# Kernel tuning notes

Hardware: AMD Instinct MI355X
Metric: run time of the kernel (lower is better)

## Reference

```python
import jax, jax.numpy as jnp
import numpy as np
from jax import lax

N = 100000      # number of nodes (== ninput)
E = 3200000     # number of edges per adjacency
NHID = 128
EPS = 1e-12     # torch F.normalize eps


def spmm(src, dst, w, x):
    # sparse adj @ x : out[i] = sum_{e: dst[e]==i} w[e] * x[src[e]]
    return jax.ops.segment_sum(w[:, None] * x[src], dst, num_segments=N)


def l2norm(x):
    # F.normalize(x, p=2, dim=1)
    n = jnp.sqrt(jnp.sum(x * x, axis=1, keepdims=True))
    return x / jnp.maximum(n, EPS)


def mlp(x, L1, bl1, L2, bl2, L3, bl3):
    # dropout == 0.0 -> identity; chunking is a memory optimization, same math
    h = jax.nn.relu(x @ L1 + bl1)
    h = jax.nn.relu(h @ L2 + bl2)
    return h @ L3 + bl3  # [N, 1]


def setup_inputs() -> dict:
    key = jax.random.key(0)
    ks = jax.random.split(key, 32)
    d = {}
    d["adj1_src"] = jax.random.randint(ks[0], (E,), 0, N, dtype=jnp.int32)
    d["adj1_dst"] = jax.random.randint(ks[1], (E,), 0, N, dtype=jnp.int32)
    d["adj1_w"] = jax.random.uniform(ks[2], (E,), dtype=jnp.float32)
    d["adj2_src"] = jax.random.randint(ks[3], (E,), 0, N, dtype=jnp.int32)
    d["adj2_dst"] = jax.random.randint(ks[4], (E,), 0, N, dtype=jnp.int32)
    d["adj2_w"] = jax.random.uniform(ks[5], (E,), dtype=jnp.float32)
    d["W1"] = jax.random.normal(ks[6], (N, NHID), dtype=jnp.float32) * 0.05
    d["b1"] = jnp.zeros((NHID,), jnp.float32)
    for i, k in zip(range(2, 7), ks[7:12]):
        d[f"W{i}"] = jax.random.normal(k, (NHID, NHID), dtype=jnp.float32) * (1.0 / np.sqrt(NHID))
        d[f"b{i}"] = jnp.zeros((NHID,), jnp.float32)
    d["L1"] = jax.random.normal(ks[12], (NHID, 2 * NHID), dtype=jnp.float32) * (1.0 / np.sqrt(NHID))
    d["bl1"] = jnp.zeros((2 * NHID,), jnp.float32)
    d["L2"] = jax.random.normal(ks[13], (2 * NHID, 2 * NHID), dtype=jnp.float32) * (1.0 / np.sqrt(2 * NHID))
    d["bl2"] = jnp.zeros((2 * NHID,), jnp.float32)
    d["L3"] = jax.random.normal(ks[14], (2 * NHID, 1), dtype=jnp.float32) * (1.0 / np.sqrt(2 * NHID))
    d["bl3"] = jnp.zeros((1,), jnp.float32)
    return d


def reference(adj1_src, adj1_dst, adj1_w, adj2_src, adj2_dst, adj2_w,
              W1, b1, W2, b2, W3, b3, W4, b4, W5, b5, W6, b6,
              L1, bl1, L2, bl2, L3, bl3):
    def branch(src, dst, w):
        x1 = l2norm(jax.nn.relu(spmm(src, dst, w, W1) + b1))
        x2 = l2norm(jax.nn.relu(spmm(src, dst, w, x1 @ W2) + b2))
        x3 = l2norm(jax.nn.relu(spmm(src, dst, w, x2 @ W3) + b3))
        x4 = l2norm(jax.nn.relu(spmm(src, dst, w, x3 @ W4) + b4))
        x5 = l2norm(jax.nn.relu(spmm(src, dst, w, x4 @ W5) + b5))
        x6 = jax.nn.relu(spmm(src, dst, w, x5 @ W6) + b6)
        x7 = lax.stop_gradient(x1 + x2 + x3 + x4 + x5 + x6)  # .detach()
        s = jnp.zeros((N, 1), jnp.float32)
        for xi in (x1, x2, x3, x4, x5):  # computed under torch.no_grad()
            s = s + lax.stop_gradient(mlp(xi, L1, bl1, L2, bl2, L3, bl3))
        s = s + mlp(x6, L1, bl1, L2, bl2, L3, bl3)
        s = s + mlp(x7, L1, bl1, L2, bl2, L3, bl3)
        return s / 7.0

    score1 = branch(adj1_src, adj1_dst, adj1_w)
    score2 = branch(adj2_src, adj2_dst, adj2_w)
    return score1 * score2
```

## Files before the change

### kernel.cpp

```cpp
#include <hip/hip_runtime.h>

#define NN 100000
#define NE 3200000
#define HID 128
#define NNH ((size_t)NN * HID)
#define CAPB 72
#define SP 13
#define FGRID 27097
#define CHE 533504
#define WROWS2 12500
#define GE8 1563

typedef __attribute__((ext_vector_type(8))) _Float16 f16x8;
typedef __attribute__((ext_vector_type(4))) _Float16 f16x4;
typedef __attribute__((ext_vector_type(4))) float f32x4;

#define SWZ(row, k) ((k) ^ (((row) & 7) << 3))

__global__ void zero_k(int* p, int n) {
    int i = blockIdx.x * 256 + threadIdx.x;
    if (i < n) p[i] = 0;
}

__global__ void scatter_xcd_k(const int* __restrict__ src, const int* __restrict__ dst,
                              const float* __restrict__ w, int* __restrict__ cnt,
                              unsigned* __restrict__ ep) {
    int wdx = blockIdx.x & 7;
    int grp = blockIdx.x >> 3;
    int lo = wdx * WROWS2;
    int hi = lo + WROWS2; if (hi > NN) hi = NN;
#pragma unroll
    for (int k = 0; k < 8; ++k) {
        int e = (grp + k * GE8) * 256 + threadIdx.x;
        if (e < NE) {
            int d = dst[e];
            if (d >= lo && d < hi) {
                int pos = atomicAdd(&cnt[d], 1);
                if (pos < CAPB) {
                    ushort hb = __builtin_bit_cast(ushort, (_Float16)w[e]);
                    ep[(size_t)d * CAPB + pos] = ((unsigned)src[e] << 15) | (unsigned)hb;
                }
            }
        }
    }
}

__global__ void convT_k(const float* __restrict__ W, _Float16* __restrict__ WT, int K, int N) {
    int idx = blockIdx.x * 256 + threadIdx.x;
    if (idx < K * N) {
        int k = idx / N, n = idx % N;
        WT[n * K + k] = (_Float16)W[idx];
    }
}

__global__ void conv4_k(const float* __restrict__ A, _Float16* __restrict__ B, int n4) {
    int i = blockIdx.x * 256 + threadIdx.x;
    if (i < n4) {
        float4 v = ((const float4*)A)[i];
        f16x4 h;
        h.x = (_Float16)v.x; h.y = (_Float16)v.y; h.z = (_Float16)v.z; h.w = (_Float16)v.w;
        ((f16x4*)B)[i] = h;
    }
}

template <bool EPI>
__device__ inline void spmm_rows4(const _Float16* __restrict__ x, const int* __restrict__ cnt,
                                  const unsigned* __restrict__ ep, const float* __restrict__ bias,
                                  _Float16* __restrict__ outx, int row0) {
    int l = threadIdx.x & 63;
    int q = l >> 4, li = l & 15;
    int row = row0 + (threadIdx.x >> 6);
    if (row >= NN) return;
    int e0 = row * CAPB;
    int deg = cnt[row];
    if (deg > CAPB) deg = CAPB;
    int e1 = e0 + deg;
    float acc[8] = {};
#pragma unroll 4
    for (int e = e0 + q; e < e1; e += 4) {
        unsigned r = ep[e];
        int s = r >> 15;
        float w = (float)__builtin_bit_cast(_Float16, (ushort)(r & 0x7FFFu));
        f16x8 v = *(const f16x8*)(x + (size_t)s * HID + li * 8);
#pragma unroll
        for (int j = 0; j < 8; ++j) acc[j] += w * (float)v[j];
    }
#pragma unroll
    for (int j = 0; j < 8; ++j) {
        acc[j] += __shfl_xor(acc[j], 16, 64);
        acc[j] += __shfl_xor(acc[j], 32, 64);
    }
    if (EPI) {
        const float4* bp = (const float4*)(bias + li * 8);
        float4 b0 = bp[0], b1 = bp[1];
        acc[0] = fmaxf(acc[0] + b0.x, 0.f); acc[1] = fmaxf(acc[1] + b0.y, 0.f);
        acc[2] = fmaxf(acc[2] + b0.z, 0.f); acc[3] = fmaxf(acc[3] + b0.w, 0.f);
        acc[4] = fmaxf(acc[4] + b1.x, 0.f); acc[5] = fmaxf(acc[5] + b1.y, 0.f);
        acc[6] = fmaxf(acc[6] + b1.z, 0.f); acc[7] = fmaxf(acc[7] + b1.w, 0.f);
        float ss = 0.f;
#pragma unroll
        for (int j = 0; j < 8; ++j) ss += acc[j] * acc[j];
        ss += __shfl_xor(ss, 1, 64);
        ss += __shfl_xor(ss, 2, 64);
        ss += __shfl_xor(ss, 4, 64);
        ss += __shfl_xor(ss, 8, 64);
        float sc = 1.0f / fmaxf(sqrtf(ss), 1e-12f);
#pragma unroll
        for (int j = 0; j < 8; ++j) acc[j] *= sc;
    }
    if (q == 0) {
        f16x8 ho;
#pragma unroll
        for (int j = 0; j < 8; ++j) ho[j] = (_Float16)acc[j];
        *(f16x8*)(outx + (size_t)row * HID + li * 8) = ho;
    }
}

template <bool EPI>
__global__ void spmm_k(const _Float16* __restrict__ x, const int* __restrict__ cnt,
                       const unsigned* __restrict__ ep, const float* __restrict__ bias,
                       _Float16* __restrict__ outx) {
    spmm_rows4<EPI>(x, cnt, ep, bias, outx, blockIdx.x * 4);
}

template <bool EPI>
__global__ void spmm_sc_k(const _Float16* __restrict__ x, const int* __restrict__ cnt,
                          const unsigned* __restrict__ ep, const float* __restrict__ bias,
                          _Float16* __restrict__ outx,
                          const int* __restrict__ src2, const int* __restrict__ dst2,
                          const float* __restrict__ w2, int* __restrict__ cnt2,
                          unsigned* __restrict__ ep2, int ebase) {
    int b = blockIdx.x;
    if (b % SP == SP - 1) {
        int e = ebase + (b / SP) * 256 + threadIdx.x;
        if (e < NE) {
            int d = dst2[e];
            int pos = atomicAdd(&cnt2[d], 1);
            if (pos < CAPB) {
                ushort hb = __builtin_bit_cast(ushort, (_Float16)w2[e]);
                ep2[(size_t)d * CAPB + pos] = ((unsigned)src2[e] << 15) | (unsigned)hb;
            }
        }
        return;
    }
    int mIdx = b - b / SP;
    spmm_rows4<EPI>(x, cnt, ep, bias, outx, mIdx * 4);
}

template <bool NORM>
__global__ __launch_bounds__(256) void trans_mlp_k(
    const _Float16* Y, const _Float16* __restrict__ WT,
    const float* __restrict__ bw, _Float16* Xo,
    const _Float16* __restrict__ L1T, const float* __restrict__ bl1,
    const _Float16* __restrict__ L2T, const float* __restrict__ bl2,
    const float* __restrict__ L3, const float* __restrict__ bl3,
    float* __restrict__ sacc) {
    __shared__ _Float16 Xs[64][128];
    __shared__ _Float16 H1s[64][256];
    __shared__ float red[4][64];
    int t = threadIdx.x;
    int w = t >> 6, l = t & 63;
    int g = l >> 4, li = l & 15;
    int rowBase = blockIdx.x * 64;

#pragma unroll
    for (int i = 0; i < 4; ++i) {
        int idx = t + i * 256;
        int r = idx >> 4, c8 = idx & 15;
        int gr = rowBase + r;
        f16x8 v = (gr < NN) ? *(const f16x8*)(Y + (size_t)gr * 128 + c8 * 8)
                            : (f16x8)(_Float16)0.f;
        *(f16x8*)&Xs[r][SWZ(r, c8 * 8)] = v;
    }
    __syncthreads();

    int cW = w * 32;
    f32x4 accw[4][2] = {};
#pragma unroll
    for (int ks = 0; ks < 4; ++ks) {
        int kb = ks * 32 + g * 8;
        f16x8 a[4];
#pragma unroll
        for (int mt = 0; mt < 4; ++mt) {
            int r = mt * 16 + li;
            a[mt] = *(const f16x8*)&Xs[r][SWZ(r, kb)];
        }
#pragma unroll
        for (int nt = 0; nt < 2; ++nt) {
            f16x8 b = *(const f16x8*)(WT + (size_t)(cW + nt * 16 + li) * 128 + kb);
#pragma unroll
            for (int mt = 0; mt < 4; ++mt)
                accw[mt][nt] = __builtin_amdgcn_mfma_f32_16x16x32_f16(a[mt], b, accw[mt][nt], 0, 0, 0);
        }
    }
    float vv[4][2][4];
    float b0 = bw[cW + li], b1v = bw[cW + 16 + li];
#pragma unroll
    for (int mt = 0; mt < 4; ++mt)
#pragma unroll
        for (int r4 = 0; r4 < 4; ++r4) {
            vv[mt][0][r4] = fmaxf(accw[mt][0][r4] + b0, 0.f);
            vv[mt][1][r4] = fmaxf(accw[mt][1][r4] + b1v, 0.f);
        }
    if (NORM) {
#pragma unroll
        for (int mt = 0; mt < 4; ++mt)
#pragma unroll
            for (int r4 = 0; r4 < 4; ++r4) {
                float ps = vv[mt][0][r4] * vv[mt][0][r4] + vv[mt][1][r4] * vv[mt][1][r4];
                ps += __shfl_xor(ps, 1, 64);
                ps += __shfl_xor(ps, 2, 64);
                ps += __shfl_xor(ps, 4, 64);
                ps += __shfl_xor(ps, 8, 64);
                if (li == 0) red[w][mt * 16 + g * 4 + r4] = ps;
            }
        __syncthreads();
        if (t < 64) {
            float s = red[0][t] + red[1][t] + red[2][t] + red[3][t];
            red[0][t] = 1.f / fmaxf(sqrtf(s), 1e-12f);
        }
        __syncthreads();
    } else {
        __syncthreads();
    }
#pragma unroll
    for (int mt = 0; mt < 4; ++mt)
#pragma unroll
        for (int r4 = 0; r4 < 4; ++r4) {
            int row = mt * 16 + g * 4 + r4;
            float sc = NORM ? red[0][row] : 1.f;
            _Float16 h0 = (_Float16)(vv[mt][0][r4] * sc);
            _Float16 h1 = (_Float16)(vv[mt][1][r4] * sc);
            Xs[row][SWZ(row, cW + li)] = h0;
            Xs[row][SWZ(row, cW + 16 + li)] = h1;
            int gr = rowBase + row;
            if (gr < NN) {
                Xo[(size_t)gr * 128 + cW + li] = h0;
                Xo[(size_t)gr * 128 + cW + 16 + li] = h1;
            }
        }
    __syncthreads();

    int cM = w * 64;
    f32x4 acc[4][4] = {};
#pragma unroll
    for (int ks = 0; ks < 4; ++ks) {
        int kb = ks * 32 + g * 8;
        f16x8 a[4];
#pragma unroll
        for (int mt = 0; mt < 4; ++mt) {
            int r = mt * 16 + li;
            a[mt] = *(const f16x8*)&Xs[r][SWZ(r, kb)];
        }
#pragma unroll
        for (int nt = 0; nt < 4; ++nt) {
            int n = cM + nt * 16 + li;
            f16x8 b = *(const f16x8*)(L1T + (size_t)n * 128 + kb);
#pragma unroll
            for (int mt = 0; mt < 4; ++mt)
                acc[mt][nt] = __builtin_amdgcn_mfma_f32_16x16x32_f16(a[mt], b, acc[mt][nt], 0, 0, 0);
        }
    }
#pragma unroll
    for (int nt = 0; nt < 4; ++nt) {
        int col = cM + nt * 16 + li;
        float bb = bl1[col];
#pragma unroll
        for (int mt = 0; mt < 4; ++mt)
#pragma unroll
            for (int r4 = 0; r4 < 4; ++r4) {
                int row = mt * 16 + g * 4 + r4;
                H1s[row][SWZ(row, col)] = (_Float16)fmaxf(acc[mt][nt][r4] + bb, 0.f);
            }
    }
    __syncthreads();

    f32x4 acc2[4][4] = {};
#pragma unroll
    for (int ks = 0; ks < 8; ++ks) {
        int kb = ks * 32 + g * 8;
        f16x8 a[4];
#pragma unroll
        for (int mt = 0; mt < 4; ++mt) {
            int r = mt * 16 + li;
            a[mt] = *(const f16x8*)&H1s[r][SWZ(r, kb)];
        }
#pragma unroll
        for (int nt = 0; nt < 4; ++nt) {
            int n = cM + nt * 16 + li;
            f16x8 b = *(const f16x8*)(L2T + (size_t)n * 256 + kb);
#pragma unroll
            for (int mt = 0; mt < 4; ++mt)
                acc2[mt][nt] = __builtin_amdgcn_mfma_f32_16x16x32_f16(a[mt], b, acc2[mt][nt], 0, 0, 0);
        }
    }
    float part[4][4] = {};
#pragma unroll
    for (int nt = 0; nt < 4; ++nt) {
        int col = cM + nt * 16 + li;
        float bb = bl2[col];
        float l3v = L3[col];
#pragma unroll
        for (int mt = 0; mt < 4; ++mt)
#pragma unroll
            for (int r4 = 0; r4 < 4; ++r4)
                part[mt][r4] += fmaxf(acc2[mt][nt][r4] + bb, 0.f) * l3v;
    }
#pragma unroll
    for (int mt = 0; mt < 4; ++mt)
#pragma unroll
        for (int r4 = 0; r4 < 4; ++r4) {
            float p = part[mt][r4];
            p += __shfl_xor(p, 1, 64);
            p += __shfl_xor(p, 2, 64);
            p += __shfl_xor(p, 4, 64);
            p += __shfl_xor(p, 8, 64);
            if (li == 0) red[w][mt * 16 + g * 4 + r4] = p;
        }
    __syncthreads();
    if (t < 64) {
        int gr = rowBase + t;
        if (gr < NN)
            sacc[gr] += red[0][t] + red[1][t] + red[2][t] + red[3][t] + bl3[0];
    }
}

template <bool SUM6, bool INIT>
__global__ __launch_bounds__(256) void mlp_fused_k(
    const _Float16* __restrict__ X,
    const _Float16* __restrict__ L1T, const float* __restrict__ bl1,
    const _Float16* __restrict__ L2T, const float* __restrict__ bl2,
    const float* __restrict__ L3, const float* __restrict__ bl3,
    float* __restrict__ sacc) {
    __shared__ _Float16 Xs[64][128];
    __shared__ _Float16 H1s[64][256];
    __shared__ float red[4][64];
    int t = threadIdx.x;
    int w = t >> 6, l = t & 63;
    int g = l >> 4, li = l & 15;
    int rowBase = blockIdx.x * 64;

#pragma unroll
    for (int i = 0; i < 4; ++i) {
        int idx = t + i * 256;
        int r = idx >> 4, c8 = idx & 15;
        int gr = rowBase + r;
        if (SUM6) {
            float s[8] = {};
            if (gr < NN) {
#pragma unroll
                for (int l6 = 0; l6 < 6; ++l6) {
                    f16x8 v = *(const f16x8*)(X + (size_t)l6 * NNH + (size_t)gr * HID + c8 * 8);
#pragma unroll
                    for (int j = 0; j < 8; ++j) s[j] += (float)v[j];
                }
            }
            f16x8 hv;
#pragma unroll
            for (int j = 0; j < 8; ++j) hv[j] = (_Float16)s[j];
            *(f16x8*)&Xs[r][SWZ(r, c8 * 8)] = hv;
        } else {
            f16x8 v = (gr < NN) ? *(const f16x8*)(X + (size_t)gr * HID + c8 * 8)
                                : (f16x8)(_Float16)0.f;
            *(f16x8*)&Xs[r][SWZ(r, c8 * 8)] = v;
        }
    }
    __syncthreads();

    int cM = w * 64;
    f32x4 acc[4][4] = {};
#pragma unroll
    for (int ks = 0; ks < 4; ++ks) {
        int kb = ks * 32 + g * 8;
        f16x8 a[4];
#pragma unroll
        for (int mt = 0; mt < 4; ++mt) {
            int r = mt * 16 + li;
            a[mt] = *(const f16x8*)&Xs[r][SWZ(r, kb)];
        }
#pragma unroll
        for (int nt = 0; nt < 4; ++nt) {
            int n = cM + nt * 16 + li;
            f16x8 b = *(const f16x8*)(L1T + (size_t)n * 128 + kb);
#pragma unroll
            for (int mt = 0; mt < 4; ++mt)
                acc[mt][nt] = __builtin_amdgcn_mfma_f32_16x16x32_f16(a[mt], b, acc[mt][nt], 0, 0, 0);
        }
    }
#pragma unroll
    for (int nt = 0; nt < 4; ++nt) {
        int col = cM + nt * 16 + li;
        float bb = bl1[col];
#pragma unroll
        for (int mt = 0; mt < 4; ++mt)
#pragma unroll
            for (int r4 = 0; r4 < 4; ++r4) {
                int row = mt * 16 + g * 4 + r4;
                H1s[row][SWZ(row, col)] = (_Float16)fmaxf(acc[mt][nt][r4] + bb, 0.f);
            }
    }
    __syncthreads();

    f32x4 acc2[4][4] = {};
#pragma unroll
    for (int ks = 0; ks < 8; ++ks) {
        int kb = ks * 32 + g * 8;
        f16x8 a[4];
#pragma unroll
        for (int mt = 0; mt < 4; ++mt) {
            int r = mt * 16 + li;
            a[mt] = *(const f16x8*)&H1s[r][SWZ(r, kb)];
        }
#pragma unroll
        for (int nt = 0; nt < 4; ++nt) {
            int n = cM + nt * 16 + li;
            f16x8 b = *(const f16x8*)(L2T + (size_t)n * 256 + kb);
#pragma unroll
            for (int mt = 0; mt < 4; ++mt)
                acc2[mt][nt] = __builtin_amdgcn_mfma_f32_16x16x32_f16(a[mt], b, acc2[mt][nt], 0, 0, 0);
        }
    }
    float part[4][4] = {};
#pragma unroll
    for (int nt = 0; nt < 4; ++nt) {
        int col = cM + nt * 16 + li;
        float bb = bl2[col];
        float l3v = L3[col];
#pragma unroll
        for (int mt = 0; mt < 4; ++mt)
#pragma unroll
            for (int r4 = 0; r4 < 4; ++r4)
                part[mt][r4] += fmaxf(acc2[mt][nt][r4] + bb, 0.f) * l3v;
    }
#pragma unroll
    for (int mt = 0; mt < 4; ++mt)
#pragma unroll
        for (int r4 = 0; r4 < 4; ++r4) {
            float p = part[mt][r4];
            p += __shfl_xor(p, 1, 64);
            p += __shfl_xor(p, 2, 64);
            p += __shfl_xor(p, 4, 64);
            p += __shfl_xor(p, 8, 64);
            if (li == 0) red[w][mt * 16 + g * 4 + r4] = p;
        }
    __syncthreads();
    if (t < 64) {
        int gr = rowBase + t;
        if (gr < NN) {
            float s = red[0][t] + red[1][t] + red[2][t] + red[3][t] + bl3[0];
            if (INIT) sacc[gr] = s; else sacc[gr] += s;
        }
    }
}

__global__ void score_store_k(const float* __restrict__ sacc, float* __restrict__ dst) {
    int i = blockIdx.x * 256 + threadIdx.x;
    if (i < NN) dst[i] = sacc[i] * (1.f / 7.f);
}

__global__ void final_mul_k(const float* __restrict__ sacc, const float* __restrict__ score1,
                            float* __restrict__ out) {
    int i = blockIdx.x * 256 + threadIdx.x;
    if (i < NN) out[i] = score1[i] * (sacc[i] * (1.f / 7.f));
}

extern "C" void kernel_launch(void* const* d_in, const int* in_sizes, int n_in,
                              void* d_out, int out_size, void* d_ws, size_t ws_size,
                              hipStream_t stream) {
    const int* asrc[2] = {(const int*)d_in[0], (const int*)d_in[3]};
    const int* adst[2] = {(const int*)d_in[1], (const int*)d_in[4]};
    const float* aw[2] = {(const float*)d_in[2], (const float*)d_in[5]};
    const float* W1 = (const float*)d_in[6];
    const float* b1 = (const float*)d_in[7];
    const float* Wk[5] = {(const float*)d_in[8], (const float*)d_in[10], (const float*)d_in[12],
                          (const float*)d_in[14], (const float*)d_in[16]};
    const float* bk[5] = {(const float*)d_in[9], (const float*)d_in[11], (const float*)d_in[13],
                          (const float*)d_in[15], (const float*)d_in[17]};
    const float* L1 = (const float*)d_in[18];
    const float* bl1 = (const float*)d_in[19];
    const float* L2 = (const float*)d_in[20];
    const float* bl2 = (const float*)d_in[21];
    const float* L3 = (const float*)d_in[22];
    const float* bl3 = (const float*)d_in[23];
    float* out = (float*)d_out;

    char* p = (char*)d_ws;
    _Float16* L1T = (_Float16*)p; p += 65536;
    _Float16* L2T = (_Float16*)p; p += 131072;
    _Float16* WkT = (_Float16*)p; p += 163840;
    _Float16* W1h = (_Float16*)p; p += NNH * 2;
    _Float16* xbuf = (_Float16*)p; p += 6 * NNH * 2;
    float* sacc = (float*)p; p += (size_t)NN * 4;
    float* score1 = (float*)p; p += (size_t)NN * 4;
    unsigned* ep1 = (unsigned*)p; p += (size_t)NN * CAPB * 4;
    unsigned* ep2 = (unsigned*)p; p += (size_t)NN * CAPB * 4;
    int* cnt1 = (int*)p; p += (size_t)NN * 4;
    int* cnt2 = (int*)p; p += (size_t)NN * 4;

    const int GE = (NE + 255) / 256;
    const int GN = (NN + 255) / 256;
    const int GS = (NN + 3) / 4;
    const int GM = (NN + 63) / 64;

    convT_k<<<(128 * 256 + 255) / 256, 256, 0, stream>>>(L1, L1T, 128, 256);
    convT_k<<<(256 * 256 + 255) / 256, 256, 0, stream>>>(L2, L2T, 256, 256);
    for (int l = 0; l < 5; ++l)
        convT_k<<<(128 * 128 + 255) / 256, 256, 0, stream>>>(Wk[l], WkT + (size_t)l * 16384, 128, 128);
    conv4_k<<<(NN * HID / 4 + 255) / 256, 256, 0, stream>>>(W1, W1h, NN * HID / 4);
    zero_k<<<GN, 256, 0, stream>>>(cnt1, NN);
    zero_k<<<GN, 256, 0, stream>>>(cnt2, NN);

    scatter_xcd_k<<<8 * GE8, 256, 0, stream>>>(asrc[0], adst[0], aw[0], cnt1, ep1);

    spmm_sc_k<true><<<FGRID, 256, 0, stream>>>(W1h, cnt1, ep1, b1, xbuf,
                                               asrc[1], adst[1], aw[1], cnt2, ep2, 0);
    mlp_fused_k<false, true><<<GM, 256, 0, stream>>>(xbuf, L1T, bl1, L2T, bl2, L3, bl3, sacc);

    for (int l = 0; l < 5; ++l) {
        _Float16* xo = xbuf + (size_t)(l + 1) * NNH;
        spmm_sc_k<false><<<FGRID, 256, 0, stream>>>(xbuf + (size_t)l * NNH, cnt1, ep1, b1, xo,
                                                    asrc[1], adst[1], aw[1], cnt2, ep2,
                                                    (l + 1) * CHE);
        if (l < 4)
            trans_mlp_k<true><<<GM, 256, 0, stream>>>(xo, WkT + (size_t)l * 16384, bk[l], xo,
                                                      L1T, bl1, L2T, bl2, L3, bl3, sacc);
        else
            trans_mlp_k<false><<<GM, 256, 0, stream>>>(xo, WkT + (size_t)l * 16384, bk[l], xo,
                                                       L1T, bl1, L2T, bl2, L3, bl3, sacc);
    }
    mlp_fused_k<true, false><<<GM, 256, 0, stream>>>(xbuf, L1T, bl1, L2T, bl2, L3, bl3, sacc);
    score_store_k<<<GN, 256, 0, stream>>>(sacc, score1);

    spmm_k<true><<<GS, 256, 0, stream>>>(W1h, cnt2, ep2, b1, xbuf);
    mlp_fused_k<false, true><<<GM, 256, 0, stream>>>(xbuf, L1T, bl1, L2T, bl2, L3, bl3, sacc);
    for (int l = 0; l < 5; ++l) {
        _Float16* xo = xbuf + (size_t)(l + 1) * NNH;
        spmm_k<false><<<GS, 256, 0, stream>>>(xbuf + (size_t)l * NNH, cnt2, ep2, b1, xo);
        if (l < 4)
            trans_mlp_k<true><<<GM, 256, 0, stream>>>(xo, WkT + (size_t)l * 16384, bk[l], xo,
                                                      L1T, bl1, L2T, bl2, L3, bl3, sacc);
        else
            trans_mlp_k<false><<<GM, 256, 0, stream>>>(xo, WkT + (size_t)l * 16384, bk[l], xo,
                                                       L1T, bl1, L2T, bl2, L3, bl3, sacc);
    }
    mlp_fused_k<true, false><<<GM, 256, 0, stream>>>(xbuf, L1T, bl1, L2T, bl2, L3, bl3, sacc);
    final_mul_k<<<GN, 256, 0, stream>>>(sacc, score1, out);
}
```

Measured before the change: 2.471 ms.

## Overlap per-layer MLP scoring with next SpMM via interleaved block roles

Moves the MLP scoring of each layer's normalized features out of the transform kernel and into the following SpMM launch, interleaving MLP blocks with SpMM (and adjacency-scatter) blocks by block-index modulo. The transform kernel becomes a lighter trans_k that only does the matmul, bias, relu and normalize. This removes the separate first MLP launch and lets the compute-heavy MLP overlap with the memory-bound gather. In exchange, grid sizing and role mapping get more complex, and shared memory for the MLP now constrains occupancy of the SpMM blocks.

```diff
diff --git a/kernel.cpp b/kernel.cpp
--- a/kernel.cpp
+++ b/kernel.cpp
@@ -10,6 +10,9 @@
 #define CHE 533504
 #define WROWS2 12500
 #define GE8 1563
+#define GM 1563
+#define G1 28692
+#define G2 26571
 
 typedef __attribute__((ext_vector_type(8))) _Float16 f16x8;
 typedef __attribute__((ext_vector_type(4))) _Float16 f16x4;
@@ -116,6 +119,115 @@
     }
 }
 
+__device__ inline void mlp_body(const _Float16* __restrict__ X, int rowBase,
+                                const _Float16* __restrict__ L1T, const float* __restrict__ bl1,
+                                const _Float16* __restrict__ L2T, const float* __restrict__ bl2,
+                                const float* __restrict__ L3, const float* __restrict__ bl3,
+                                float* __restrict__ sacc, int initF) {
+    __shared__ _Float16 Xs[64][128];
+    __shared__ _Float16 H1s[64][256];
+    __shared__ float red[4][64];
+    int t = threadIdx.x;
+    int w = t >> 6, l = t & 63;
+    int g = l >> 4, li = l & 15;
+
+#pragma unroll
+    for (int i = 0; i < 4; ++i) {
+        int idx = t + i * 256;
+        int r = idx >> 4, c8 = idx & 15;
+        int gr = rowBase + r;
+        f16x8 v = (gr < NN) ? *(const f16x8*)(X + (size_t)gr * HID + c8 * 8)
+                            : (f16x8)(_Float16)0.f;
+        *(f16x8*)&Xs[r][SWZ(r, c8 * 8)] = v;
+    }
+    __syncthreads();
+
+    int cM = w * 64;
+    f32x4 acc[4][4] = {};
+#pragma unroll
+    for (int ks = 0; ks < 4; ++ks) {
+        int kb = ks * 32 + g * 8;
+        f16x8 a[4];
+#pragma unroll
+        for (int mt = 0; mt < 4; ++mt) {
+            int r = mt * 16 + li;
+            a[mt] = *(const f16x8*)&Xs[r][SWZ(r, kb)];
+        }
+#pragma unroll
+        for (int nt = 0; nt < 4; ++nt) {
+            int n = cM + nt * 16 + li;
+            f16x8 b = *(const f16x8*)(L1T + (size_t)n * 128 + kb);
+#pragma unroll
+            for (int mt = 0; mt < 4; ++mt)
+                acc[mt][nt] = __builtin_amdgcn_mfma_f32_16x16x32_f16(a[mt], b, acc[mt][nt], 0, 0, 0);
+        }
+    }
+#pragma unroll
+    for (int nt = 0; nt < 4; ++nt) {
+        int col = cM + nt * 16 + li;
+        float bb = bl1[col];
+#pragma unroll
+        for (int mt = 0; mt < 4; ++mt)
+#pragma unroll
+            for (int r4 = 0; r4 < 4; ++r4) {
+                int row = mt * 16 + g * 4 + r4;
+                H1s[row][SWZ(row, col)] = (_Float16)fmaxf(acc[mt][nt][r4] + bb, 0.f);
+            }
+    }
+    __syncthreads();
+
+    f32x4 acc2[4][4] = {};
+#pragma unroll
+    for (int ks = 0; ks < 8; ++ks) {
+        int kb = ks * 32 + g * 8;
+        f16x8 a[4];
+#pragma unroll
+        for (int mt = 0; mt < 4; ++mt) {
+            int r = mt * 16 + li;
+            a[mt] = *(const f16x8*)&H1s[r][SWZ(r, kb)];
+        }
+#pragma unroll
+        for (int nt = 0; nt < 4; ++nt) {
+            int n = cM + nt * 16 + li;
+            f16x8 b = *(const f16x8*)(L2T + (size_t)n * 256 + kb);
+#pragma unroll
+            for (int mt = 0; mt < 4; ++mt)
+                acc2[mt][nt] = __builtin_amdgcn_mfma_f32_16x16x32_f16(a[mt], b, acc2[mt][nt], 0, 0, 0);
+        }
+    }
+    float part[4][4] = {};
+#pragma unroll
+    for (int nt = 0; nt < 4; ++nt) {
+        int col = cM + nt * 16 + li;
+        float bb = bl2[col];
+        float l3v = L3[col];
+#pragma unroll
+        for (int mt = 0; mt < 4; ++mt)
+#pragma unroll
+            for (int r4 = 0; r4 < 4; ++r4)
+                part[mt][r4] += fmaxf(acc2[mt][nt][r4] + bb, 0.f) * l3v;
+    }
+#pragma unroll
+    for (int mt = 0; mt < 4; ++mt)
+#pragma unroll
+        for (int r4 = 0; r4 < 4; ++r4) {
+            float p = part[mt][r4];
+            p += __shfl_xor(p, 1, 64);
+            p += __shfl_xor(p, 2, 64);
+            p += __shfl_xor(p, 4, 64);
+            p += __shfl_xor(p, 8, 64);
+            if (li == 0) red[w][mt * 16 + g * 4 + r4] = p;
+        }
+    __syncthreads();
+    if (t < 64) {
+        int gr = rowBase + t;
+        if (gr < NN) {
+            float s = red[0][t] + red[1][t] + red[2][t] + red[3][t] + bl3[0];
+            if (initF) sacc[gr] = s; else sacc[gr] += s;
+        }
+    }
+}
+
 template <bool EPI>
 __global__ void spmm_k(const _Float16* __restrict__ x, const int* __restrict__ cnt,
                        const unsigned* __restrict__ ep, const float* __restrict__ bias,
@@ -147,6 +259,143 @@
     spmm_rows4<EPI>(x, cnt, ep, bias, outx, mIdx * 4);
 }
 
+__global__ __launch_bounds__(256) void fused3_k(
+    const _Float16* __restrict__ x, const int* __restrict__ cnt,
+    const unsigned* __restrict__ ep, _Float16* __restrict__ outx,
+    const int* __restrict__ src2, const int* __restrict__ dst2,
+    const float* __restrict__ w2, int* __restrict__ cnt2,
+    unsigned* __restrict__ ep2, int ebase,
+    const _Float16* __restrict__ Xp, int initF,
+    const _Float16* __restrict__ L1T, const float* __restrict__ bl1,
+    const _Float16* __restrict__ L2T, const float* __restrict__ bl2,
+    const float* __restrict__ L3, const float* __restrict__ bl3,
+    float* __restrict__ sacc) {
+    int b = blockIdx.x;
+    int m18 = b % 18;
+    if (m18 == 9) {
+        int midx = b / 18;
+        if (midx < GM) mlp_body(Xp, midx * 64, L1T, bl1, L2T, bl2, L3, bl3, sacc, initF);
+        return;
+    }
+    int nm = b / 18 + (m18 > 9 ? 1 : 0);
+    int rank = b - nm;
+    if (rank % 13 == 12) {
+        int e = ebase + (rank / 13) * 256 + threadIdx.x;
+        if (e < NE) {
+            int d = dst2[e];
+            int pos = atomicAdd(&cnt2[d], 1);
+            if (pos < CAPB) {
+                ushort hb = __builtin_bit_cast(ushort, (_Float16)w2[e]);
+                ep2[(size_t)d * CAPB + pos] = ((unsigned)src2[e] << 15) | (unsigned)hb;
+            }
+        }
+        return;
+    }
+    int sIdx = rank - rank / 13;
+    spmm_rows4<false>(x, cnt, ep, nullptr, outx, sIdx * 4);
+}
+
+__global__ __launch_bounds__(256) void fused2_k(
+    const _Float16* __restrict__ x, const int* __restrict__ cnt,
+    const unsigned* __restrict__ ep, _Float16* __restrict__ outx,
+    const _Float16* __restrict__ Xp, int initF,
+    const _Float16* __restrict__ L1T, const float* __restrict__ bl1,
+    const _Float16* __restrict__ L2T, const float* __restrict__ bl2,
+    const float* __restrict__ L3, const float* __restrict__ bl3,
+    float* __restrict__ sacc) {
+    int b = blockIdx.x;
+    int m17 = b % 17;
+    if (m17 == 8) {
+        int midx = b / 17;
+        if (midx < GM) mlp_body(Xp, midx * 64, L1T, bl1, L2T, bl2, L3, bl3, sacc, initF);
+        return;
+    }
+    int nm = b / 17 + (m17 > 8 ? 1 : 0);
+    int sIdx = b - nm;
+    spmm_rows4<false>(x, cnt, ep, nullptr, outx, sIdx * 4);
+}
+
+__global__ __launch_bounds__(256) void trans_k(
+    const _Float16* Y, const _Float16* __restrict__ WT,
+    const float* __restrict__ bw, _Float16* Xo) {
+    __shared__ _Float16 Xs[64][128];
+    __shared__ float red[64];
+    int t = threadIdx.x;
+    int w = t >> 6, l = t & 63;
+    int g = l >> 4, li = l & 15;
+    int rowBase = blockIdx.x * 64;
+
+#pragma unroll
+    for (int i = 0; i < 4; ++i) {
+        int idx = t + i * 256;
+        int r = idx >> 4, c8 = idx & 15;
+        int gr = rowBase + r;
+        f16x8 v = (gr < NN) ? *(const f16x8*)(Y + (size_t)gr * 128 + c8 * 8)
+                            : (f16x8)(_Float16)0.f;
+        *(f16x8*)&Xs[r][SWZ(r, c8 * 8)] = v;
+    }
+    __syncthreads();
+
+    int cW = w * 32;
+    f32x4 accw[4][2] = {};
+#pragma unroll
+    for (int ks = 0; ks < 4; ++ks) {
+        int kb = ks * 32 + g * 8;
+        f16x8 a[4];
+#pragma unroll
+        for (int mt = 0; mt < 4; ++mt) {
+            int r = mt * 16 + li;
+            a[mt] = *(const f16x8*)&Xs[r][SWZ(r, kb)];
+        }
+#pragma unroll
+        for (int nt = 0; nt < 2; ++nt) {
+            f16x8 b = *(const f16x8*)(WT + (size_t)(cW + nt * 16 + li) * 128 + kb);
+#pragma unroll
+            for (int mt = 0; mt < 4; ++mt)
+                accw[mt][nt] = __builtin_amdgcn_mfma_f32_16x16x32_f16(a[mt], b, accw[mt][nt], 0, 0, 0);
+        }
+    }
+    float vv[4][2][4];
+    float b0 = bw[cW + li], b1v = bw[cW + 16 + li];
+#pragma unroll
+    for (int mt = 0; mt < 4; ++mt)
+#pragma unroll
+        for (int r4 = 0; r4 < 4; ++r4) {
+            vv[mt][0][r4] = fmaxf(accw[mt][0][r4] + b0, 0.f);
+            vv[mt][1][r4] = fmaxf(accw[mt][1][r4] + b1v, 0.f);
+        }
+    __shared__ float psum[4][64];
+#pragma unroll
+    for (int mt = 0; mt < 4; ++mt)
+#pragma unroll
+        for (int r4 = 0; r4 < 4; ++r4) {
+            float ps = vv[mt][0][r4] * vv[mt][0][r4] + vv[mt][1][r4] * vv[mt][1][r4];
+            ps += __shfl_xor(ps, 1, 64);
+            ps += __shfl_xor(ps, 2, 64);
+            ps += __shfl_xor(ps, 4, 64);
+            ps += __shfl_xor(ps, 8, 64);
+            if (li == 0) psum[w][mt * 16 + g * 4 + r4] = ps;
+        }
+    __syncthreads();
+    if (t < 64) {
+        float s = psum[0][t] + psum[1][t] + psum[2][t] + psum[3][t];
+        red[t] = 1.f / fmaxf(sqrtf(s), 1e-12f);
+    }
+    __syncthreads();
+#pragma unroll
+    for (int mt = 0; mt < 4; ++mt)
+#pragma unroll
+        for (int r4 = 0; r4 < 4; ++r4) {
+            int row = mt * 16 + g * 4 + r4;
+            float sc = red[row];
+            int gr = rowBase + row;
+            if (gr < NN) {
+                Xo[(size_t)gr * 128 + cW + li] = (_Float16)(vv[mt][0][r4] * sc);
+                Xo[(size_t)gr * 128 + cW + 16 + li] = (_Float16)(vv[mt][1][r4] * sc);
+            }
+        }
+}
+
 template <bool NORM>
 __global__ __launch_bounds__(256) void trans_mlp_k(
     const _Float16* Y, const _Float16* __restrict__ WT,
@@ -325,8 +574,7 @@
     }
 }
 
-template <bool SUM6, bool INIT>
-__global__ __launch_bounds__(256) void mlp_fused_k(
+__global__ __launch_bounds__(256) void mlp_sum6_k(
     const _Float16* __restrict__ X,
     const _Float16* __restrict__ L1T, const float* __restrict__ bl1,
     const _Float16* __restrict__ L2T, const float* __restrict__ bl2,
@@ -345,25 +593,19 @@
         int idx = t + i * 256;
         int r = idx >> 4, c8 = idx & 15;
         int gr = rowBase + r;
-        if (SUM6) {
-            float s[8] = {};
-            if (gr < NN) {
-#pragma unroll
-                for (int l6 = 0; l6 < 6; ++l6) {
-                    f16x8 v = *(const f16x8*)(X + (size_t)l6 * NNH + (size_t)gr * HID + c8 * 8);
-#pragma unroll
-                    for (int j = 0; j < 8; ++j) s[j] += (float)v[j];
-                }
-            }
-            f16x8 hv;
-#pragma unroll
-            for (int j = 0; j < 8; ++j) hv[j] = (_Float16)s[j];
-            *(f16x8*)&Xs[r][SWZ(r, c8 * 8)] = hv;
-        } else {
-            f16x8 v = (gr < NN) ? *(const f16x8*)(X + (size_t)gr * HID + c8 * 8)
-                                : (f16x8)(_Float16)0.f;
-            *(f16x8*)&Xs[r][SWZ(r, c8 * 8)] = v;
-        }
+        float s[8] = {};
+        if (gr < NN) {
+#pragma unroll
+            for (int l6 = 0; l6 < 6; ++l6) {
+                f16x8 v = *(const f16x8*)(X + (size_t)l6 * NNH + (size_t)gr * HID + c8 * 8);
+#pragma unroll
+                for (int j = 0; j < 8; ++j) s[j] += (float)v[j];
+            }
+        }
+        f16x8 hv;
+#pragma unroll
+        for (int j = 0; j < 8; ++j) hv[j] = (_Float16)s[j];
+        *(f16x8*)&Xs[r][SWZ(r, c8 * 8)] = hv;
     }
     __syncthreads();
 
@@ -446,10 +688,8 @@
     __syncthreads();
     if (t < 64) {
         int gr = rowBase + t;
-        if (gr < NN) {
-            float s = red[0][t] + red[1][t] + red[2][t] + red[3][t] + bl3[0];
-            if (INIT) sacc[gr] = s; else sacc[gr] += s;
-        }
+        if (gr < NN)
+            sacc[gr] += red[0][t] + red[1][t] + red[2][t] + red[3][t] + bl3[0];
     }
 }
 
@@ -500,7 +740,6 @@
     const int GE = (NE + 255) / 256;
     const int GN = (NN + 255) / 256;
     const int GS = (NN + 3) / 4;
-    const int GM = (NN + 63) / 64;
 
     convT_k<<<(128 * 256 + 255) / 256, 256, 0, stream>>>(L1, L1T, 128, 256);
     convT_k<<<(256 * 256 + 255) / 256, 256, 0, stream>>>(L2, L2T, 256, 256);
@@ -511,38 +750,35 @@
     zero_k<<<GN, 256, 0, stream>>>(cnt2, NN);
 
     scatter_xcd_k<<<8 * GE8, 256, 0, stream>>>(asrc[0], adst[0], aw[0], cnt1, ep1);
-
     spmm_sc_k<true><<<FGRID, 256, 0, stream>>>(W1h, cnt1, ep1, b1, xbuf,
                                                asrc[1], adst[1], aw[1], cnt2, ep2, 0);
-    mlp_fused_k<false, true><<<GM, 256, 0, stream>>>(xbuf, L1T, bl1, L2T, bl2, L3, bl3, sacc);
-
     for (int l = 0; l < 5; ++l) {
         _Float16* xo = xbuf + (size_t)(l + 1) * NNH;
-        spmm_sc_k<false><<<FGRID, 256, 0, stream>>>(xbuf + (size_t)l * NNH, cnt1, ep1, b1, xo,
-                                                    asrc[1], adst[1], aw[1], cnt2, ep2,
-                                                    (l + 1) * CHE);
+        fused3_k<<<G1, 256, 0, stream>>>(xbuf + (size_t)l * NNH, cnt1, ep1, xo,
+                                         asrc[1], adst[1], aw[1], cnt2, ep2, (l + 1) * CHE,
+                                         xbuf + (size_t)l * NNH, (l == 0) ? 1 : 0,
+                                         L1T, bl1, L2T, bl2, L3, bl3, sacc);
         if (l < 4)
-            trans_mlp_k<true><<<GM, 256, 0, stream>>>(xo, WkT + (size_t)l * 16384, bk[l], xo,
-                                                      L1T, bl1, L2T, bl2, L3, bl3, sacc);
+            trans_k<<<GM, 256, 0, stream>>>(xo, WkT + (size_t)l * 16384, bk[l], xo);
         else
             trans_mlp_k<false><<<GM, 256, 0, stream>>>(xo, WkT + (size_t)l * 16384, bk[l], xo,
                                                        L1T, bl1, L2T, bl2, L3, bl3, sacc);
     }
-    mlp_fused_k<true, false><<<GM, 256, 0, stream>>>(xbuf, L1T, bl1, L2T, bl2, L3, bl3, sacc);
+    mlp_sum6_k<<<GM, 256, 0, stream>>>(xbuf, L1T, bl1, L2T, bl2, L3, bl3, sacc);
     score_store_k<<<GN, 256, 0, stream>>>(sacc, score1);
 
     spmm_k<true><<<GS, 256, 0, stream>>>(W1h, cnt2, ep2, b1, xbuf);
-    mlp_fused_k<false, true><<<GM, 256, 0, stream>>>(xbuf, L1T, bl1, L2T, bl2, L3, bl3, sacc);
     for (int l = 0; l < 5; ++l) {
         _Float16* xo = xbuf + (size_t)(l + 1) * NNH;
-        spmm_k<false><<<GS, 256, 0, stream>>>(xbuf + (size_t)l * NNH, cnt2, ep2, b1, xo);
+        fused2_k<<<G2, 256, 0, stream>>>(xbuf + (size_t)l * NNH, cnt2, ep2, xo,
+                                         xbuf + (size_t)l * NNH, (l == 0) ? 1 : 0,
+                                         L1T, bl1, L2T, bl2, L3, bl3, sacc);
         if (l < 4)
-            trans_mlp_k<true><<<GM, 256, 0, stream>>>(xo, WkT + (size_t)l * 16384, bk[l], xo,
-                                                      L1T, bl1, L2T, bl2, L3, bl3, sacc);
+            trans_k<<<GM, 256, 0, stream>>>(xo, WkT + (size_t)l * 16384, bk[l], xo);
         else
             trans_mlp_k<false><<<GM, 256, 0, stream>>>(xo, WkT + (size_t)l * 16384, bk[l], xo,
                                                        L1T, bl1, L2T, bl2, L3, bl3, sacc);
     }
-    mlp_fused_k<true, false><<<GM, 256, 0, stream>>>(xbuf, L1T, bl1, L2T, bl2, L3, bl3, sacc);
+    mlp_sum6_k<<<GM, 256, 0, stream>>>(xbuf, L1T, bl1, L2T, bl2, L3, bl3, sacc);
     final_mul_k<<<GN, 256, 0, stream>>>(sacc, score1, out);
 }
```

Result: slower. 5.516 ms (+123.2%).
